# Performance work log

Measured on AMD Instinct MI355X. Metric: run time of the kernel, lower is better.

## Reference

```python
import jax, jax.numpy as jnp
import numpy as np

D_MODEL = 1024
N_HEADS = 16
D_H = D_MODEL // N_HEADS
B, S = 2, 2048


def setup_inputs() -> dict:
    key = jax.random.key(0)
    ks = jax.random.split(key, 12)
    s = 1.0 / np.sqrt(D_MODEL)
    inp = {
        "Q": jax.random.normal(ks[0], (B, S, D_MODEL), jnp.float32),
        "K": jax.random.normal(ks[1], (B, S, D_MODEL), jnp.float32),
        "V": jax.random.normal(ks[2], (B, S, D_MODEL), jnp.float32),
        # causal mask: True means masked out (matches masked_fill semantics)
        "masked": jnp.broadcast_to(~jnp.tril(jnp.ones((S, S), bool)), (B, S, S)),
        "WQ_w": jax.random.uniform(ks[3], (D_MODEL, D_MODEL), jnp.float32, -s, s),
        "WQ_b": jax.random.uniform(ks[4], (D_MODEL,), jnp.float32, -s, s),
        "WK_w": jax.random.uniform(ks[5], (D_MODEL, D_MODEL), jnp.float32, -s, s),
        "WK_b": jax.random.uniform(ks[6], (D_MODEL,), jnp.float32, -s, s),
        "WV_w": jax.random.uniform(ks[7], (D_MODEL, D_MODEL), jnp.float32, -s, s),
        "WV_b": jax.random.uniform(ks[8], (D_MODEL,), jnp.float32, -s, s),
        "Wo_w": jax.random.uniform(ks[9], (D_MODEL, D_MODEL), jnp.float32, -s, s),
        "Wo_b": jax.random.uniform(ks[10], (D_MODEL,), jnp.float32, -s, s),
    }
    return inp


def reference(Q, K, V, masked, WQ_w, WQ_b, WK_w, WK_b, WV_w, WV_b, Wo_w, Wo_b):
    b = Q.shape[0]
    # torch Linear: y = x @ W^T + b
    def split_heads(x):
        return x.reshape(b, -1, N_HEADS, D_H).transpose(0, 2, 1, 3)  # [B,H,S,d_h]

    q = split_heads(Q @ WQ_w.T + WQ_b)
    k = split_heads(K @ WK_w.T + WK_b)
    v = split_heads(V @ WV_w.T + WV_b)

    scores = jnp.einsum("bhqd,bhkd->bhqk", q, k) / np.sqrt(D_H)
    scores = jnp.where(masked[:, None, :, :], jnp.float32(-1e9), scores)
    attn = jax.nn.softmax(scores, axis=-1)
    ctx = jnp.einsum("bhqk,bhkd->bhqd", attn, v)  # [B,H,S,d_h]
    ctx = ctx.transpose(0, 2, 1, 3).reshape(b, -1, N_HEADS * D_H)
    return ctx @ Wo_w.T + Wo_b
```

## Files before the change

kernel.cpp:

```cpp
#include <hip/hip_runtime.h>
#include <hip/hip_bf16.h>
#include <math.h>


typedef __bf16 bf16_t;
typedef bf16_t bf16x8 __attribute__((ext_vector_type(8)));
typedef bf16_t bf16x4 __attribute__((ext_vector_type(4)));
typedef float f32x4 __attribute__((ext_vector_type(4)));

#define MFMA16(a, b, c) __builtin_amdgcn_mfma_f32_16x16x32_bf16(a, b, c, 0, 0, 0)

constexpr int S_LEN = 2048;
constexpr int DMODEL = 1024;
constexpr int DHEAD = 64;
constexpr int MTOT = 2 * S_LEN;
constexpr size_t NQ = (size_t)MTOT * DMODEL;
constexpr size_t NW = (size_t)DMODEL * DMODEL;
constexpr float ESC = 0.18033688011112042f;

__device__ __forceinline__ void load_lds16(const void* g, void* l) {
  __builtin_amdgcn_global_load_lds((const __attribute__((address_space(1))) void*)g,
                                   (__attribute__((address_space(3))) void*)l, 16, 0, 0);
}

__global__ __launch_bounds__(256) void convert_all(
    const float* __restrict__ Q, const float* __restrict__ K, const float* __restrict__ V,
    const float* __restrict__ W0, const float* __restrict__ W1, const float* __restrict__ W2,
    const float* __restrict__ W3, bf16_t* __restrict__ dst) {
  const size_t i = ((size_t)blockIdx.x * 256 + threadIdx.x) * 4;
  const float* s;
  size_t off = i;
  if (off < NQ) { s = Q; }
  else if (off < 2 * NQ) { s = K; off -= NQ; }
  else if (off < 3 * NQ) { s = V; off -= 2 * NQ; }
  else {
    off -= 3 * NQ;
    if (off < NW) { s = W0; }
    else if (off < 2 * NW) { s = W1; off -= NW; }
    else if (off < 3 * NW) { s = W2; off -= 2 * NW; }
    else { s = W3; off -= 3 * NW; }
  }
  const float4 v4 = *(const float4*)(s + off);
  bf16x4 b;
  b[0] = (bf16_t)v4.x; b[1] = (bf16_t)v4.y; b[2] = (bf16_t)v4.z; b[3] = (bf16_t)v4.w;
  *(bf16x4*)(dst + i) = b;
}

template <int BK>
__device__ __forceinline__ void gemm_loop(const bf16_t* __restrict__ Ab,
                                          const bf16_t* __restrict__ Wb,
                                          bf16_t* As, bf16_t* Ws,
                                          f32x4 (&acc)[4][4], int wave, int lane) {
  constexpr int CH = BK / 8;
  constexpr int RPI = 64 / CH;
  constexpr int IPW = BK / 16;
  const int col = lane & 15, quad = lane >> 4;
  const int wm = (wave >> 1) * 64, wn = (wave & 1) * 64;
  const int srow = lane / CH;
  const int sch = lane % CH;

  for (int k0 = 0; k0 < 1024; k0 += BK) {
    __syncthreads();
#pragma unroll
    for (int i = 0; i < IPW; i++) {
      const int rbase = (i * 4 + wave) * RPI;
      const int g = sch ^ ((rbase + srow) & 7);
      load_lds16(Ab + (size_t)(rbase + srow) * 1024 + k0 + g * 8, As + rbase * BK);
      load_lds16(Wb + (size_t)(rbase + srow) * 1024 + k0 + g * 8, Ws + rbase * BK);
    }
    __syncthreads();
#pragma unroll
    for (int kc = 0; kc < BK / 32; kc++) {
      const int slot = (kc * 4 + quad) ^ (col & 7);
      bf16x8 af[4], wf[4];
#pragma unroll
      for (int i = 0; i < 4; i++) af[i] = *(const bf16x8*)&As[(wm + i * 16 + col) * BK + slot * 8];
#pragma unroll
      for (int j = 0; j < 4; j++) wf[j] = *(const bf16x8*)&Ws[(wn + j * 16 + col) * BK + slot * 8];
#pragma unroll
      for (int i = 0; i < 4; i++)
#pragma unroll
        for (int j = 0; j < 4; j++) acc[i][j] = MFMA16(af[i], wf[j], acc[i][j]);
    }
  }
}

__global__ __launch_bounds__(256, 3) void gemm_qkv(const bf16_t* __restrict__ Abase,
                                                   const bf16_t* __restrict__ Wbase,
                                                   const float* __restrict__ b0,
                                                   const float* __restrict__ b1,
                                                   const float* __restrict__ b2,
                                                   bf16_t* __restrict__ obase) {
  __shared__ bf16_t As[128 * 64];
  __shared__ bf16_t Ws[128 * 64];
  const int z = blockIdx.z;
  const int bm = blockIdx.x * 128, bn = blockIdx.y * 128;
  const int lane = threadIdx.x & 63, wave = threadIdx.x >> 6;
  const int col = lane & 15, quad = lane >> 4;
  const int wm = (wave >> 1) * 64, wn = (wave & 1) * 64;

  f32x4 acc[4][4];
#pragma unroll
  for (int i = 0; i < 4; i++)
#pragma unroll
    for (int j = 0; j < 4; j++)
#pragma unroll
      for (int r = 0; r < 4; r++) acc[i][j][r] = 0.f;

  const bf16_t* A = Abase + z * NQ + (size_t)bm * 1024;
  const bf16_t* W = Wbase + z * NW + (size_t)bn * 1024;
  const float* bias = (z == 0) ? b0 : ((z == 1) ? b1 : b2);
  bf16_t* out = obase + z * NQ;

  gemm_loop<64>(A, W, As, Ws, acc, wave, lane);

  const float esc = (z == 0) ? ESC : 1.0f;
#pragma unroll
  for (int i = 0; i < 4; i++) {
#pragma unroll
    for (int j = 0; j < 4; j++) {
      const int n = bn + wn + j * 16 + col;
      const float bv = bias[n];
      const int h = n >> 6, dh = n & 63;
      if (z < 2) {
#pragma unroll
        for (int r = 0; r < 4; r++) {
          const int m = bm + wm + i * 16 + quad * 4 + r;
          const int b = m >> 11, s = m & 2047;
          out[((size_t)((b * 16 + h) * S_LEN + s) << 6) | dh] =
              (bf16_t)((acc[i][j][r] + bv) * esc);
        }
      } else {
        const int m0 = bm + wm + i * 16 + quad * 4;
        const int b = m0 >> 11, s0 = m0 & 2047;
        bf16x4 p4;
#pragma unroll
        for (int r = 0; r < 4; r++) p4[r] = (bf16_t)(acc[i][j][r] + bv);
        *(bf16x4*)&out[(((size_t)((b * 16 + h) * DHEAD + dh)) << 11) | s0] = p4;
      }
    }
  }
}

__global__ __launch_bounds__(256) void gemm_out(const bf16_t* __restrict__ A,
                                                const bf16_t* __restrict__ W,
                                                const float* __restrict__ bias,
                                                float* __restrict__ out) {
  __shared__ bf16_t As[128 * 128];
  __shared__ bf16_t Ws[128 * 128];
  const int bm = blockIdx.x * 128, bn = blockIdx.y * 128;
  const int lane = threadIdx.x & 63, wave = threadIdx.x >> 6;
  const int col = lane & 15, quad = lane >> 4;
  const int wm = (wave >> 1) * 64, wn = (wave & 1) * 64;

  f32x4 acc[4][4];
#pragma unroll
  for (int i = 0; i < 4; i++)
#pragma unroll
    for (int j = 0; j < 4; j++)
#pragma unroll
      for (int r = 0; r < 4; r++) acc[i][j][r] = 0.f;

  gemm_loop<128>(A + (size_t)bm * 1024, W + (size_t)bn * 1024, As, Ws, acc, wave, lane);

#pragma unroll
  for (int i = 0; i < 4; i++)
#pragma unroll
    for (int j = 0; j < 4; j++) {
      const int n = bn + wn + j * 16 + col;
      const float bv = bias[n];
#pragma unroll
      for (int r = 0; r < 4; r++) {
        const int m = bm + wm + i * 16 + quad * 4 + r;
        out[(size_t)m * DMODEL + n] = acc[i][j][r] + bv;
      }
    }
}

constexpr int PP = 136;

__global__ __launch_bounds__(256, 2) void attn(const bf16_t* __restrict__ q,
                                               const bf16_t* __restrict__ k,
                                               const bf16_t* __restrict__ vT,
                                               bf16_t* __restrict__ ctx) {
  const int bh = blockIdx.x;
  const int p = blockIdx.y;
  const int tA = p, tB = 15 - p;
  const int lane = threadIdx.x & 63, wave = threadIdx.x >> 6;
  const int col = lane & 15, quad = lane >> 4;

  __shared__ bf16_t Ks[128 * 64];
  __shared__ bf16_t Vs[64 * 128];
  __shared__ bf16_t Ps[4][32 * PP];

  const bf16_t* kbh = k + (size_t)bh * S_LEN * DHEAD;
  const bf16_t* vbh = vT + (size_t)bh * DHEAD * S_LEN;

  const int k_srow = lane >> 3, k_g = (lane & 7) ^ k_srow;
  const int v_row = lane >> 4, v_sl = lane & 15;

  bf16x8 aq[2][2];
  f32x4 o[2][4];
  float lsum[2];

  for (int it = 0; it <= 16; ++it) {
    const bool onA = (it <= tA);
    const int T = onA ? tA : tB;
    const int c = onA ? it : it - (tA + 1);

    if (c == 0) {
      const bf16_t* qb = q + ((size_t)bh * S_LEN + T * 128 + wave * 32 + col) * DHEAD;
#pragma unroll
      for (int qf = 0; qf < 2; qf++) {
        aq[qf][0] = *(const bf16x8*)(qb + qf * 16 * DHEAD + quad * 8);
        aq[qf][1] = *(const bf16x8*)(qb + qf * 16 * DHEAD + 32 + quad * 8);
      }
#pragma unroll
      for (int qf = 0; qf < 2; qf++) {
        lsum[qf] = 0.f;
#pragma unroll
        for (int db = 0; db < 4; db++)
#pragma unroll
          for (int r = 0; r < 4; r++) o[qf][db][r] = 0.f;
      }
    }

    __syncthreads();
#pragma unroll
    for (int i = 0; i < 4; i++) {
      const int rbase = wave * 32 + i * 8;
      load_lds16(kbh + (size_t)(c * 128 + rbase + k_srow) * DHEAD + k_g * 8, &Ks[rbase * 64]);
    }
#pragma unroll
    for (int i = 0; i < 4; i++) {
      const int dbase = wave * 16 + i * 4;
      const int d = dbase + v_row;
      const int g = v_sl ^ (d & 7);
      load_lds16(vbh + (size_t)d * S_LEN + c * 128 + g * 8, &Vs[dbase * 128]);
    }
    __syncthreads();

    f32x4 sacc[2][8];
#pragma unroll
    for (int qf = 0; qf < 2; qf++)
#pragma unroll
      for (int nb = 0; nb < 8; nb++)
#pragma unroll
        for (int r = 0; r < 4; r++) sacc[qf][nb][r] = 0.f;
#pragma unroll
    for (int kc = 0; kc < 2; kc++) {
      const int slot = (kc * 4 + quad) ^ (col & 7);
#pragma unroll
      for (int nb = 0; nb < 8; nb++) {
        const bf16x8 bk = *(const bf16x8*)&Ks[(nb * 16 + col) * 64 + slot * 8];
#pragma unroll
        for (int qf = 0; qf < 2; qf++) sacc[qf][nb] = MFMA16(bk, aq[qf][kc], sacc[qf][nb]);
      }
    }

    const bool diag = (c == T);
#pragma unroll
    for (int qf = 0; qf < 2; qf++) {
      const int ql = wave * 32 + qf * 16 + col;
#pragma unroll
      for (int nb = 0; nb < 8; nb++) {
        bf16x4 p4;
#pragma unroll
        for (int r = 0; r < 4; r++) {
          const int keyl = nb * 16 + quad * 4 + r;
          float pv = exp2f(sacc[qf][nb][r]);
          if (diag && keyl > ql) pv = 0.f;
          lsum[qf] += pv;
          p4[r] = (bf16_t)pv;
        }
        *(bf16x4*)&Ps[wave][(qf * 16 + col) * PP + nb * 16 + quad * 4] = p4;
      }
    }

#pragma unroll
    for (int kc = 0; kc < 4; kc++) {
      const int slotv = (kc * 4 + quad) ^ (col & 7);
      bf16x8 pa[2];
#pragma unroll
      for (int qf = 0; qf < 2; qf++)
        pa[qf] = *(const bf16x8*)&Ps[wave][(qf * 16 + col) * PP + kc * 32 + quad * 8];
#pragma unroll
      for (int db = 0; db < 4; db++) {
        const bf16x8 bv = *(const bf16x8*)&Vs[(db * 16 + col) * 128 + slotv * 8];
#pragma unroll
        for (int qf = 0; qf < 2; qf++) o[qf][db] = MFMA16(bv, pa[qf], o[qf][db]);
      }
    }

    if (c == T) {
      const int b = bh >> 4, h = bh & 15;
#pragma unroll
      for (int qf = 0; qf < 2; qf++) {
        float l = lsum[qf];
        l += __shfl_xor(l, 16);
        l += __shfl_xor(l, 32);
        const float inv = 1.f / l;
        const int qg = T * 128 + wave * 32 + qf * 16 + col;
        bf16_t* cb = ctx + ((size_t)(b * S_LEN + qg)) * DMODEL + h * DHEAD;
#pragma unroll
        for (int db = 0; db < 4; db++) {
          bf16x4 o4;
#pragma unroll
          for (int r = 0; r < 4; r++) o4[r] = (bf16_t)(o[qf][db][r] * inv);
          *(bf16x4*)&cb[db * 16 + quad * 4] = o4;
        }
      }
    }
  }
}

extern "C" void kernel_launch(void* const* d_in, const int* in_sizes, int n_in,
                              void* d_out, int out_size, void* d_ws, size_t ws_size,
                              hipStream_t stream) {
  const float* Q = (const float*)d_in[0];
  const float* K = (const float*)d_in[1];
  const float* V = (const float*)d_in[2];
  const float* WQw = (const float*)d_in[4];
  const float* WQb = (const float*)d_in[5];
  const float* WKw = (const float*)d_in[6];
  const float* WKb = (const float*)d_in[7];
  const float* WVw = (const float*)d_in[8];
  const float* WVb = (const float*)d_in[9];
  const float* Wow = (const float*)d_in[10];
  const float* Wob = (const float*)d_in[11];

  bf16_t* base = (bf16_t*)d_ws;
  bf16_t* Wc = base + 3 * NQ;
  bf16_t* qp = base + 3 * NQ + 4 * NW;
  bf16_t* ctx = base;

  const size_t total = 3 * NQ + 4 * NW;
  convert_all<<<dim3((unsigned)(total / 4 / 256)), dim3(256), 0, stream>>>(
      Q, K, V, WQw, WKw, WVw, Wow, base);

  gemm_qkv<<<dim3(32, 8, 3), dim3(256), 0, stream>>>(base, Wc, WQb, WKb, WVb, qp);
  attn<<<dim3(32, 8), dim3(256), 0, stream>>>(qp, qp + NQ, qp + 2 * NQ, ctx);
  gemm_out<<<dim3(32, 8), dim3(256), 0, stream>>>(ctx, Wc + 3 * NW, Wob, (float*)d_out);
}
```

Measured before the change: 244.9 us.

## Double-buffer attention K/V tiles, split query rows across blocks, shrink out-GEMM tiles

The attention kernel now double-buffers K and V tiles in LDS so the loads for the next chunk overlap compute on the current one. Each block now handles 64 query rows (16 per wave) rather than 128, doubling the grid via a z dimension. The P scratch buffer uses an XOR swizzle in place of padding. The output GEMM switches to 64x128 tiles with its own inline loop and two blocks per CU, doubling block count for better occupancy. The cost is K/V being reloaded by twice as many blocks, and lower reuse per block.

New measurement: 232.0 us. -5.3%, faster.

```diff
diff --git a/kernel.cpp b/kernel.cpp
--- a/kernel.cpp
+++ b/kernel.cpp
@@ -142,29 +142,61 @@
   }
 }
 
-__global__ __launch_bounds__(256) void gemm_out(const bf16_t* __restrict__ A,
-                                                const bf16_t* __restrict__ W,
-                                                const float* __restrict__ bias,
-                                                float* __restrict__ out) {
-  __shared__ bf16_t As[128 * 128];
-  __shared__ bf16_t Ws[128 * 128];
-  const int bm = blockIdx.x * 128, bn = blockIdx.y * 128;
+__global__ __launch_bounds__(256, 2) void gemm_out(const bf16_t* __restrict__ A,
+                                                   const bf16_t* __restrict__ W,
+                                                   const float* __restrict__ bias,
+                                                   float* __restrict__ out) {
+  __shared__ bf16_t As[64 * 64];
+  __shared__ bf16_t Ws[128 * 64];
+  const int bm = blockIdx.x * 64, bn = blockIdx.y * 128;
   const int lane = threadIdx.x & 63, wave = threadIdx.x >> 6;
   const int col = lane & 15, quad = lane >> 4;
-  const int wm = (wave >> 1) * 64, wn = (wave & 1) * 64;
-
-  f32x4 acc[4][4];
-#pragma unroll
-  for (int i = 0; i < 4; i++)
+  const int wm = (wave >> 1) * 32, wn = (wave & 1) * 64;
+
+  f32x4 acc[2][4];
+#pragma unroll
+  for (int i = 0; i < 2; i++)
 #pragma unroll
     for (int j = 0; j < 4; j++)
 #pragma unroll
       for (int r = 0; r < 4; r++) acc[i][j][r] = 0.f;
 
-  gemm_loop<128>(A + (size_t)bm * 1024, W + (size_t)bn * 1024, As, Ws, acc, wave, lane);
-
-#pragma unroll
-  for (int i = 0; i < 4; i++)
+  const int srow = lane >> 3, s7 = lane & 7;
+  const bf16_t* Ab = A + (size_t)bm * 1024;
+  const bf16_t* Wb = W + (size_t)bn * 1024;
+
+  for (int k0 = 0; k0 < 1024; k0 += 64) {
+    __syncthreads();
+#pragma unroll
+    for (int i = 0; i < 2; i++) {
+      const int rbase = (i * 4 + wave) * 8;
+      const int g = s7 ^ srow;
+      load_lds16(Ab + (size_t)(rbase + srow) * 1024 + k0 + g * 8, As + rbase * 64);
+    }
+#pragma unroll
+    for (int i = 0; i < 4; i++) {
+      const int rbase = (i * 4 + wave) * 8;
+      const int g = s7 ^ srow;
+      load_lds16(Wb + (size_t)(rbase + srow) * 1024 + k0 + g * 8, Ws + rbase * 64);
+    }
+    __syncthreads();
+#pragma unroll
+    for (int kc = 0; kc < 2; kc++) {
+      const int slot = (kc * 4 + quad) ^ (col & 7);
+      bf16x8 af[2], wf[4];
+#pragma unroll
+      for (int i = 0; i < 2; i++) af[i] = *(const bf16x8*)&As[(wm + i * 16 + col) * 64 + slot * 8];
+#pragma unroll
+      for (int j = 0; j < 4; j++) wf[j] = *(const bf16x8*)&Ws[(wn + j * 16 + col) * 64 + slot * 8];
+#pragma unroll
+      for (int i = 0; i < 2; i++)
+#pragma unroll
+        for (int j = 0; j < 4; j++) acc[i][j] = MFMA16(af[i], wf[j], acc[i][j]);
+    }
+  }
+
+#pragma unroll
+  for (int i = 0; i < 2; i++)
 #pragma unroll
     for (int j = 0; j < 4; j++) {
       const int n = bn + wn + j * 16 + col;
@@ -176,8 +208,6 @@
       }
     }
 }
-
-constexpr int PP = 136;
 
 __global__ __launch_bounds__(256, 2) void attn(const bf16_t* __restrict__ q,
                                                const bf16_t* __restrict__ k,
@@ -185,132 +215,123 @@
                                                bf16_t* __restrict__ ctx) {
   const int bh = blockIdx.x;
   const int p = blockIdx.y;
+  const int half = blockIdx.z;
   const int tA = p, tB = 15 - p;
   const int lane = threadIdx.x & 63, wave = threadIdx.x >> 6;
   const int col = lane & 15, quad = lane >> 4;
 
-  __shared__ bf16_t Ks[128 * 64];
-  __shared__ bf16_t Vs[64 * 128];
-  __shared__ bf16_t Ps[4][32 * PP];
+  __shared__ bf16_t Ks[2][128 * 64];
+  __shared__ bf16_t Vs[2][64 * 128];
+  __shared__ bf16_t Ps[4][16 * 128];
 
   const bf16_t* kbh = k + (size_t)bh * S_LEN * DHEAD;
   const bf16_t* vbh = vT + (size_t)bh * DHEAD * S_LEN;
 
   const int k_srow = lane >> 3, k_g = (lane & 7) ^ k_srow;
   const int v_row = lane >> 4, v_sl = lane & 15;
-
-  bf16x8 aq[2][2];
-  f32x4 o[2][4];
-  float lsum[2];
+  const int qrow = half * 64 + wave * 16 + col;
+
+  auto stage = [&](int c, int b) {
+#pragma unroll
+    for (int i = 0; i < 4; i++) {
+      const int rbase = (wave * 4 + i) * 8;
+      load_lds16(kbh + (size_t)(c * 128 + rbase + k_srow) * DHEAD + k_g * 8,
+                 &Ks[b][rbase * 64]);
+    }
+#pragma unroll
+    for (int i = 0; i < 4; i++) {
+      const int dbase = (wave * 4 + i) * 4;
+      const int d = dbase + v_row;
+      const int g = v_sl ^ (d & 7);
+      load_lds16(vbh + (size_t)d * S_LEN + c * 128 + g * 8, &Vs[b][dbase * 128]);
+    }
+  };
+
+  bf16x8 aq[2];
+  f32x4 o[4];
+  float lsum = 0.f;
+  int buf = 0;
+
+  stage(0, 0);
 
   for (int it = 0; it <= 16; ++it) {
     const bool onA = (it <= tA);
     const int T = onA ? tA : tB;
-    const int c = onA ? it : it - (tA + 1);
+    const int c = onA ? it : it - tA - 1;
 
     if (c == 0) {
-      const bf16_t* qb = q + ((size_t)bh * S_LEN + T * 128 + wave * 32 + col) * DHEAD;
-#pragma unroll
-      for (int qf = 0; qf < 2; qf++) {
-        aq[qf][0] = *(const bf16x8*)(qb + qf * 16 * DHEAD + quad * 8);
-        aq[qf][1] = *(const bf16x8*)(qb + qf * 16 * DHEAD + 32 + quad * 8);
-      }
-#pragma unroll
-      for (int qf = 0; qf < 2; qf++) {
-        lsum[qf] = 0.f;
-#pragma unroll
-        for (int db = 0; db < 4; db++)
-#pragma unroll
-          for (int r = 0; r < 4; r++) o[qf][db][r] = 0.f;
-      }
-    }
-
-    __syncthreads();
-#pragma unroll
-    for (int i = 0; i < 4; i++) {
-      const int rbase = wave * 32 + i * 8;
-      load_lds16(kbh + (size_t)(c * 128 + rbase + k_srow) * DHEAD + k_g * 8, &Ks[rbase * 64]);
-    }
-#pragma unroll
-    for (int i = 0; i < 4; i++) {
-      const int dbase = wave * 16 + i * 4;
-      const int d = dbase + v_row;
-      const int g = v_sl ^ (d & 7);
-      load_lds16(vbh + (size_t)d * S_LEN + c * 128 + g * 8, &Vs[dbase * 128]);
-    }
-    __syncthreads();
-
-    f32x4 sacc[2][8];
-#pragma unroll
-    for (int qf = 0; qf < 2; qf++)
-#pragma unroll
-      for (int nb = 0; nb < 8; nb++)
-#pragma unroll
-        for (int r = 0; r < 4; r++) sacc[qf][nb][r] = 0.f;
+      const bf16_t* qb = q + ((size_t)bh * S_LEN + T * 128 + qrow) * DHEAD;
+      aq[0] = *(const bf16x8*)(qb + quad * 8);
+      aq[1] = *(const bf16x8*)(qb + 32 + quad * 8);
+      lsum = 0.f;
+#pragma unroll
+      for (int db = 0; db < 4; db++)
+#pragma unroll
+        for (int r = 0; r < 4; r++) o[db][r] = 0.f;
+    }
+
+    __syncthreads();
+
+    if (it < 16) stage((it + 1 <= tA) ? it + 1 : it - tA, buf ^ 1);
+
+    f32x4 sacc[8];
+#pragma unroll
+    for (int nb = 0; nb < 8; nb++)
+#pragma unroll
+      for (int r = 0; r < 4; r++) sacc[nb][r] = 0.f;
 #pragma unroll
     for (int kc = 0; kc < 2; kc++) {
-      const int slot = (kc * 4 + quad) ^ (col & 7);
+      const int sl = (kc * 4 + quad) ^ (col & 7);
 #pragma unroll
       for (int nb = 0; nb < 8; nb++) {
-        const bf16x8 bk = *(const bf16x8*)&Ks[(nb * 16 + col) * 64 + slot * 8];
-#pragma unroll
-        for (int qf = 0; qf < 2; qf++) sacc[qf][nb] = MFMA16(bk, aq[qf][kc], sacc[qf][nb]);
+        const bf16x8 bk = *(const bf16x8*)&Ks[buf][(nb * 16 + col) * 64 + sl * 8];
+        sacc[nb] = MFMA16(bk, aq[kc], sacc[nb]);
       }
     }
 
     const bool diag = (c == T);
 #pragma unroll
-    for (int qf = 0; qf < 2; qf++) {
-      const int ql = wave * 32 + qf * 16 + col;
-#pragma unroll
-      for (int nb = 0; nb < 8; nb++) {
-        bf16x4 p4;
-#pragma unroll
-        for (int r = 0; r < 4; r++) {
-          const int keyl = nb * 16 + quad * 4 + r;
-          float pv = exp2f(sacc[qf][nb][r]);
-          if (diag && keyl > ql) pv = 0.f;
-          lsum[qf] += pv;
-          p4[r] = (bf16_t)pv;
-        }
-        *(bf16x4*)&Ps[wave][(qf * 16 + col) * PP + nb * 16 + quad * 4] = p4;
-      }
+    for (int nb = 0; nb < 8; nb++) {
+      bf16x4 p4;
+#pragma unroll
+      for (int r = 0; r < 4; r++) {
+        float pv = exp2f(sacc[nb][r]);
+        if (diag && (nb * 16 + quad * 4 + r) > qrow) pv = 0.f;
+        lsum += pv;
+        p4[r] = (bf16_t)pv;
+      }
+      const int sl = (2 * nb + (quad >> 1)) ^ (col & 7);
+      *(bf16x4*)&Ps[wave][col * 128 + sl * 8 + (quad & 1) * 4] = p4;
     }
 
 #pragma unroll
     for (int kc = 0; kc < 4; kc++) {
-      const int slotv = (kc * 4 + quad) ^ (col & 7);
-      bf16x8 pa[2];
-#pragma unroll
-      for (int qf = 0; qf < 2; qf++)
-        pa[qf] = *(const bf16x8*)&Ps[wave][(qf * 16 + col) * PP + kc * 32 + quad * 8];
+      const int sl = (4 * kc + quad) ^ (col & 7);
+      const bf16x8 pa = *(const bf16x8*)&Ps[wave][col * 128 + sl * 8];
 #pragma unroll
       for (int db = 0; db < 4; db++) {
-        const bf16x8 bv = *(const bf16x8*)&Vs[(db * 16 + col) * 128 + slotv * 8];
-#pragma unroll
-        for (int qf = 0; qf < 2; qf++) o[qf][db] = MFMA16(bv, pa[qf], o[qf][db]);
+        const bf16x8 bv = *(const bf16x8*)&Vs[buf][(db * 16 + col) * 128 + sl * 8];
+        o[db] = MFMA16(bv, pa, o[db]);
       }
     }
 
     if (c == T) {
+      float l = lsum;
+      l += __shfl_xor(l, 16);
+      l += __shfl_xor(l, 32);
+      const float inv = 1.f / l;
       const int b = bh >> 4, h = bh & 15;
-#pragma unroll
-      for (int qf = 0; qf < 2; qf++) {
-        float l = lsum[qf];
-        l += __shfl_xor(l, 16);
-        l += __shfl_xor(l, 32);
-        const float inv = 1.f / l;
-        const int qg = T * 128 + wave * 32 + qf * 16 + col;
-        bf16_t* cb = ctx + ((size_t)(b * S_LEN + qg)) * DMODEL + h * DHEAD;
-#pragma unroll
-        for (int db = 0; db < 4; db++) {
-          bf16x4 o4;
-#pragma unroll
-          for (int r = 0; r < 4; r++) o4[r] = (bf16_t)(o[qf][db][r] * inv);
-          *(bf16x4*)&cb[db * 16 + quad * 4] = o4;
-        }
-      }
-    }
+      const int qg = T * 128 + qrow;
+      bf16_t* cb = ctx + ((size_t)(b * S_LEN + qg)) * DMODEL + h * DHEAD;
+#pragma unroll
+      for (int db = 0; db < 4; db++) {
+        bf16x4 o4;
+#pragma unroll
+        for (int r = 0; r < 4; r++) o4[r] = (bf16_t)(o[db][r] * inv);
+        *(bf16x4*)&cb[db * 16 + quad * 4] = o4;
+      }
+    }
+    buf ^= 1;
   }
 }
 
@@ -339,6 +360,6 @@
       Q, K, V, WQw, WKw, WVw, Wow, base);
 
   gemm_qkv<<<dim3(32, 8, 3), dim3(256), 0, stream>>>(base, Wc, WQb, WKb, WVb, qp);
-  attn<<<dim3(32, 8), dim3(256), 0, stream>>>(qp, qp + NQ, qp + 2 * NQ, ctx);
-  gemm_out<<<dim3(32, 8), dim3(256), 0, stream>>>(ctx, Wc + 3 * NW, Wob, (float*)d_out);
-}
+  attn<<<dim3(32, 8, 2), dim3(256), 0, stream>>>(qp, qp + NQ, qp + 2 * NQ, ctx);
+  gemm_out<<<dim3(64, 8), dim3(256), 0, stream>>>(ctx, Wc + 3 * NW, Wob, (float*)d_out);
+}
```
